# Kernel tuning notes

Measured on AMD Instinct MI355X. Metric: run time of the kernel, lower is better.

Reference implementation:

```python
import jax, jax.numpy as jnp
import numpy as np

LP, LQ, B, D0, H = 128, 128, 64, 150, 150
D = 2 * D0  # in_size after self-concatenation


def setup_inputs() -> dict:
    key = jax.random.key(0)
    ks = jax.random.split(key, 12)
    s = 0.08  # weight scale to keep tanh/sigmoid out of hard saturation
    return {
        "Up": jax.random.normal(ks[0], (LP, B, D0), jnp.float32),
        "Uq": jax.random.normal(ks[1], (LQ, B, D0), jnp.float32),
        "Wp": jax.random.normal(ks[2], (H, D), jnp.float32) * s,
        "Wq": jax.random.normal(ks[3], (H, D), jnp.float32) * s,
        "Wv": jax.random.normal(ks[4], (H, H), jnp.float32) * s,
        "Wg": jax.random.normal(ks[5], (2 * D, 2 * D), jnp.float32) * s,
        "V": jax.random.normal(ks[6], (B, H), jnp.float32) * s,
        "v0": jax.random.normal(ks[7], (B, H), jnp.float32) * s,
        "W_ih": jax.random.normal(ks[8], (3 * H, 2 * D), jnp.float32) * s,
        "W_hh": jax.random.normal(ks[9], (3 * H, H), jnp.float32) * s,
        "b_ih": jax.random.normal(ks[10], (3 * H,), jnp.float32) * s,
        "b_hh": jax.random.normal(ks[11], (3 * H,), jnp.float32) * s,
    }


def reference(Up, Uq, Wp, Wq, Wv, Wg, V, v0, W_ih, W_hh, b_ih, b_hh):
    # self-concat of features, as in the original forward
    Upc = jnp.concatenate([Up, Up], axis=2)  # (LP, B, D)
    Uqc = jnp.concatenate([Uq, Uq], axis=2)  # (LQ, B, D)
    # Wq @ Uq is loop-invariant in the original; hoist it (same math)
    Wuq = jnp.einsum('lbd,hd->lbh', Uqc, Wq)  # (LQ, B, H)

    def step(v, up_i):
        # up_i: (B, D); v: (B, H)
        wup = up_i @ Wp.T                                   # (B, H)
        x = jnp.tanh(wup[None] + Wuq + (v @ Wv.T)[None])    # (LQ, B, H)
        s = jnp.einsum('lbh,bh->bl', x, V)                  # (B, LQ)
        a = jax.nn.softmax(s, axis=1)
        c = jnp.einsum('bl,lbd->bd', a, Uqc)                # (B, D)
        r = jnp.concatenate([up_i, c], axis=1)              # (B, 2D)
        r = jax.nn.sigmoid(r @ Wg.T) * r                    # gated input
        # PyTorch GRUCell math
        gi = r @ W_ih.T + b_ih                              # (B, 3H)
        gh = v @ W_hh.T + b_hh                              # (B, 3H)
        i_r, i_z, i_n = jnp.split(gi, 3, axis=1)
        h_r, h_z, h_n = jnp.split(gh, 3, axis=1)
        rr = jax.nn.sigmoid(i_r + h_r)
        zz = jax.nn.sigmoid(i_z + h_z)
        n = jnp.tanh(i_n + rr * h_n)
        h = (1.0 - zz) * n + zz * v
        return h, h

    _, vs = jax.lax.scan(step, v0, Upc)  # vs: (LP, B, H)
    return vs  # dropout in eval mode = identity
```

## Files before the change

kernel.cpp:

```cpp
#include <hip/hip_runtime.h>
#include <hip/hip_fp16.h>

typedef _Float16 h2_t __attribute__((ext_vector_type(2)));

__device__ __forceinline__ float dot2f(int w, int x, float acc) {
#if __has_builtin(__builtin_amdgcn_fdot2)
  return __builtin_amdgcn_fdot2(__builtin_bit_cast(h2_t, w),
                                __builtin_bit_cast(h2_t, x), acc, false);
#else
  h2_t a = __builtin_bit_cast(h2_t, w);
  h2_t b = __builtin_bit_cast(h2_t, x);
  return acc + (float)a[0] * (float)b[0] + (float)a[1] * (float)b[1];
#endif
}

__device__ __forceinline__ float rcp_f(float x) {
#if __has_builtin(__builtin_amdgcn_rcpf)
  return __builtin_amdgcn_rcpf(x);
#else
  return 1.0f / x;
#endif
}

__device__ __forceinline__ float fast_tanh(float x) {
  float e = exp2f(x * 2.885390082f);
  return 1.0f - 2.0f * rcp_f(e + 1.0f);
}
__device__ __forceinline__ float fast_sigmoid(float x) {
  return rcp_f(1.0f + exp2f(x * -1.442695041f));
}
__device__ __forceinline__ int packh2(float a, float b) {
  h2_t h;
  h[0] = (_Float16)a;
  h[1] = (_Float16)b;
  return __builtin_bit_cast(int, h);
}

__device__ __forceinline__ int ldi_coh(const int* p) {
  return __hip_atomic_load((int*)p, __ATOMIC_RELAXED, __HIP_MEMORY_SCOPE_AGENT);
}
__device__ __forceinline__ float ldf_coh(const float* p) {
  return __hip_atomic_load((float*)p, __ATOMIC_RELAXED,
                           __HIP_MEMORY_SCOPE_AGENT);
}
__device__ __forceinline__ void sti_coh(int* p, int v) {
  __hip_atomic_store(p, v, __ATOMIC_RELAXED, __HIP_MEMORY_SCOPE_AGENT);
}
__device__ __forceinline__ void stf_coh(float* p, float v) {
  __hip_atomic_store(p, v, __ATOMIC_RELAXED, __HIP_MEMORY_SCOPE_AGENT);
}

#define DOTC(W, X, A)                                                          \
  {                                                                            \
    int4 _x = (X);                                                             \
    A = dot2f((W).x, _x.x, A);                                                 \
    A = dot2f((W).y, _x.y, A);                                                 \
    A = dot2f((W).z, _x.z, A);                                                 \
    A = dot2f((W).w, _x.w, A);                                                 \
  }

__global__ void prep_weights(const float* __restrict__ Wp,
                             const float* __restrict__ Wv,
                             const float* __restrict__ Wg,
                             const float* __restrict__ Wih,
                             const float* __restrict__ Whh,
                             __half* __restrict__ oMa, __half* __restrict__ oWg,
                             __half* __restrict__ oWih,
                             __half* __restrict__ oWhh, int* __restrict__ flags,
                             int* __restrict__ payload) {
  if (blockIdx.x == 0) {
    for (int j = threadIdx.x; j < 1024; j += 256) flags[j] = 0;
  }
  int idx = blockIdx.x * 256 + threadIdx.x;
  const int NMa = 150 * 304, NWg = 600 * 304, NWih = 900 * 304,
            NWhh = 452 * 152;
  if (idx < NMa) {
    int r = idx / 304, c = idx % 304;
    float v = 0.f;
    if (c < 150)
      v = Wp[r * 300 + c] + Wp[r * 300 + 150 + c];
    else if (c >= 152 && c < 302)
      v = Wv[r * 150 + (c - 152)];
    oMa[(c >> 3) * 1200 + r * 8 + (c & 7)] = __float2half(v);
    return;
  }
  idx -= NMa;
  if (idx < NWg) {
    int r = idx / 304, c = idx % 304;
    float v = 0.f;
    if (c < 150)
      v = Wg[r * 600 + c] + Wg[r * 600 + 150 + c];
    else if (c >= 152 && c < 302) {
      int d = c - 152;
      v = Wg[r * 600 + 300 + d] + Wg[r * 600 + 450 + d];
    }
    oWg[(c >> 3) * 4800 + r * 8 + (c & 7)] = __float2half(v);
    return;
  }
  idx -= NWg;
  if (idx < NWih) {
    int s = idx / 304, c = idx % 304;
    int r = s >> 1, off = (s & 1) * 300;
    float v = (c < 300) ? Wih[r * 600 + off + c] : 0.f;
    oWih[(c >> 3) * 7200 + s * 8 + (c & 7)] = __float2half(v);
    return;
  }
  idx -= NWih;
  if (idx < NWhh) {
    int r = idx / 152, c = idx % 152;
    float v = (r < 450 && c < 150) ? Whh[r * 150 + c] : 0.f;
    oWhh[(c >> 3) * 3616 + r * 8 + (c & 7)] = __float2half(v);
  }
}

__global__ __launch_bounds__(256) void prep_wuq(const float* __restrict__ Uq,
                                                const float* __restrict__ Wq,
                                                __half* __restrict__ oWuq,
                                                __half* __restrict__ oUqh) {
  __shared__ float sUql[64 * 150];
  const int l = blockIdx.x, tid = threadIdx.x;
  for (int idx = tid; idx < 9600; idx += 256) sUql[idx] = Uq[l * 9600 + idx];
  __syncthreads();
  for (int idx = tid; idx < 64 * 152; idx += 256) {
    int bb = idx / 152, d = idx % 152;
    float v = (d < 150) ? sUql[bb * 150 + d] : 0.f;
    oUqh[(size_t)bb * 19456 + l * 152 + d] = __float2half(v);
  }
  if (tid < 152) {
    const int h = tid;
    if (h < 150) {
      float wq[150];
#pragma unroll
      for (int d = 0; d < 150; ++d)
        wq[d] = Wq[h * 300 + d] + Wq[h * 300 + 150 + d];
      for (int bb = 0; bb < 64; ++bb) {
        float acc = 0.f;
#pragma unroll
        for (int d = 0; d < 150; ++d) acc += wq[d] * sUql[bb * 150 + d];
        oWuq[(size_t)bb * 19456 + l * 152 + h] = __float2half(acc);
      }
    } else {
      for (int bb = 0; bb < 64; ++bb)
        oWuq[(size_t)bb * 19456 + l * 152 + h] = __float2half(0.f);
    }
  }
}

__device__ __forceinline__ void post_and_wait(int* f4, int q, int target) {
  __syncthreads();
  if (threadIdx.x == 0) sti_coh(&f4[q], target);
  if (threadIdx.x < 4) {
    int spins = 0;
    while (ldi_coh(&f4[threadIdx.x]) < target && ++spins < (1 << 20)) {
      __builtin_amdgcn_s_sleep(1);
    }
  }
  __syncthreads();
}

__global__ __launch_bounds__(1024, 1) void pq_main(
    const float* __restrict__ Up, const float* __restrict__ V,
    const float* __restrict__ v0, const float* __restrict__ b_ih,
    const float* __restrict__ b_hh, const int* __restrict__ gWuq,
    const __half* __restrict__ gUqh, const int* __restrict__ gMa,
    const int* __restrict__ gWg, const int* __restrict__ gWih,
    const int* __restrict__ gWhh, int* __restrict__ flags,
    int* __restrict__ payload, float* __restrict__ out) {
  __shared__ __align__(16) float sTV[304];
  __shared__ __align__(16) float sV[152];
  __shared__ __align__(16) float sGh[456];
  __shared__ __align__(16) float sS[128];
  __shared__ __align__(16) float sSS[4];
  __shared__ __align__(16) float sC0[152];
  __shared__ __align__(16) float sCp[608];
  __shared__ __align__(16) float sU[152];
  __shared__ __align__(16) float sv_[152];
  __shared__ __align__(16) int sXd[152];
  __shared__ __align__(16) int svh[76];
  __shared__ __align__(16) int sRgh[304];
  __shared__ __align__(16) float sGi[456];
  __shared__ __align__(16) float sBih[456];
  __shared__ __align__(16) float sBhh[456];
  extern __shared__ __align__(16) int dynlds[];
  int* sWuq = dynlds;
  __half* sUqh = (__half*)(dynlds + 9728);

  const int t = threadIdx.x;
  const int c = blockIdx.x & 63;
  const int q = blockIdx.x >> 6;
  const int b = c;

  int* myflags = flags + c * 16;
  int* pl = payload + c * 4096;
  float* plS = (float*)pl;
  float* plGh = (float*)(pl + 512);
  float* plGi = (float*)(pl + 1024);

  const int4* MaT4 = (const int4*)gMa;
  const int4* WgT4 = (const int4*)gWg;
  const int4* WihT4 = (const int4*)gWih;
  const int4* WhhT4 = (const int4*)gWhh;

  const int baseR = 113 * q - (q == 3 ? 1 : 0);
  const int cntR = (q < 2) ? 113 : 112;
  const int c_lo = (q == 0) ? 0 : (q == 1) ? 18 : (q == 2) ? 38 : 56;
  const int c_hi = (q == 0) ? 18 : (q == 1) ? 37 : (q == 2) ? 56 : 75;

  int4 a0, a1, a2, a3, a4, a5, a6, a7, a8, a9;
  int4 b0, b1, b2, b3, b4, b5, b6, b7, b8, b9;
  {
    const int4* p;
    int nr, sub, step, nch, row;
    if (t < 152) {
      p = MaT4; nr = 150; step = 4; nch = 38;
      sub = t & 3; row = 38 * q + (t >> 2);
      if (row > 149) row = 149;
    } else if (t < 378) {
      p = WhhT4; nr = 452; step = 2; nch = 19;
      int u2 = t - 152; sub = u2 & 1; row = baseR + (u2 >> 1);
    } else if (t >= 384 && t < 984) {
      p = WgT4; nr = 600; step = 4; nch = 38;
      int u2 = t - 384; sub = u2 & 3; row = 150 * q + (u2 >> 2);
    } else {
      p = MaT4; nr = 150; step = 4; nch = 38; sub = 0; row = 0;
    }
#define LDA(i)                                                                 \
  {                                                                            \
    int cc = sub + step * (i);                                                 \
    if (cc > nch - 1) cc = nch - 1;                                            \
    a##i = p[cc * nr + row];                                                   \
  }
    LDA(0) LDA(1) LDA(2) LDA(3) LDA(4) LDA(5) LDA(6) LDA(7) LDA(8) LDA(9)
#undef LDA
  }
  {
    int row = (t < 900) ? (t >> 1) : 0;
    int sub = (t < 900) ? (t & 1) : 0;
#define LDB(i)                                                                 \
  {                                                                            \
    int cq = c_lo + sub + 2 * (i);                                             \
    if (cq > c_hi) cq = c_hi;                                                  \
    int hf = (cq >= 38) ? 1 : 0;                                               \
    int cc = cq - 38 * hf;                                                     \
    b##i = WihT4[cc * 900 + 2 * row + hf];                                     \
  }
    LDB(0) LDB(1) LDB(2) LDB(3) LDB(4) LDB(5) LDB(6) LDB(7) LDB(8) LDB(9)
#undef LDB
  }

  for (int idx = t; idx < 9728; idx += 1024) sWuq[idx] = gWuq[b * 9728 + idx];
  {
    const int* gU2 = (const int*)(gUqh + (size_t)b * 19456);
    int* sU2 = (int*)sUqh;
    for (int idx = t; idx < 9728; idx += 1024) sU2[idx] = gU2[idx];
  }
  if (t < 150) {
    sV[t] = V[b * 150 + t];
    float v_ = v0[b * 150 + t];
    sv_[t] = v_;
    float vn = __shfl_down(v_, 1);
    if (!(t & 1)) svh[t >> 1] = packh2(v_, vn);
    float u_ = Up[b * 150 + t];
    sU[t] = u_;
    float un = __shfl_down(u_, 1);
    if (!(t & 1)) sXd[t >> 1] = packh2(u_, un);
  }
  for (int idx = t; idx < 450; idx += 1024) {
    sBih[idx] = b_ih[idx];
    sBhh[idx] = b_hh[idx];
  }
  if (t < 304) {
    sRgh[t] = 0;
    sTV[t] = 0.f;
  }
  if (t == 0) {
    svh[75] = 0;
    sXd[75] = 0;
    sXd[151] = 0;
    sV[150] = 0.f;
    sV[151] = 0.f;
  }
  const int4* sXd4 = (const int4*)sXd;
  const int4* svh4 = (const int4*)svh;
  const int4* sRgh4 = (const int4*)sRgh;
  const int c_lq = t / 150;
  const int c_d0 = t - c_lq * 150;
  __syncthreads();

#pragma unroll 1
  for (int i = 0; i < 128; ++i) {
    float unext = 0.f;
    if (t >= 640 && t < 790) {
      int ii = (i < 127) ? (i + 1) : 127;
      unext = Up[ii * 9600 + b * 150 + (t - 640)];
    }

    if (t < 152) {
      int rl = t >> 2, sub = t & 3;
      float acc0 = 0.f, acc1 = 0.f;
#define MAD(i2, A)                                                             \
  {                                                                            \
    int cc = sub + 4 * (i2);                                                   \
    if (cc < 38) {                                                             \
      int4 x = (cc < 19) ? sXd4[cc] : svh4[cc - 19];                           \
      DOTC(a##i2, x, A)                                                        \
    }                                                                          \
  }
      MAD(0, acc0) MAD(1, acc1) MAD(2, acc0) MAD(3, acc1) MAD(4, acc0)
      MAD(5, acc1) MAD(6, acc0) MAD(7, acc1) MAD(8, acc0) MAD(9, acc1)
#undef MAD
      float acc = acc0 + acc1;
      acc += __shfl_xor(acc, 1);
      acc += __shfl_xor(acc, 2);
      float accN = __shfl_down(acc, 4);
      if (sub == 0 && !(rl & 1)) {
        int w = 19 * q + (rl >> 1);
        int h = 38 * q + rl;
        float4 tv;
        tv.x = acc;
        tv.y = accN;
        tv.z = sV[h];
        tv.w = sV[h + 1];
        ((float4*)sTV)[w] = tv;
      }
    } else if (t < 378) {
      int u2 = t - 152;
      int rl = u2 >> 1, sub = u2 & 1;
      int r = baseR + rl;
      float acc0 = 0.f, acc1 = 0.f;
#define HHD(i2, A)                                                             \
  {                                                                            \
    int cc = sub + 2 * (i2);                                                   \
    if (cc < 19) DOTC(a##i2, svh4[cc], A)                                      \
  }
      HHD(0, acc0) HHD(1, acc1) HHD(2, acc0) HHD(3, acc1) HHD(4, acc0)
      HHD(5, acc1) HHD(6, acc0) HHD(7, acc1) HHD(8, acc0) HHD(9, acc1)
#undef HHD
      float acc = acc0 + acc1;
      acc += __shfl_xor(acc, 1);
      if (sub == 0 && rl < cntR) stf_coh(&plGh[r], acc + sBhh[r]);
    }
    __syncthreads();

    {
      const int l = t >> 3, sub = t & 7;
      const int base = l * 76;
      float acc = 0.f;
#pragma unroll
      for (int k = 0; k < 3; ++k) {
        int wl = sub + 8 * k;
        if (wl < 19) {
          int w = 19 * q + wl;
          int qq = sWuq[base + w];
          float4 tv = ((const float4*)sTV)[w];
          h2_t hq = __builtin_bit_cast(h2_t, qq);
          float x0 = (float)hq[0] + tv.x;
          float x1 = (float)hq[1] + tv.y;
          acc += fast_tanh(x0) * tv.z;
          acc += fast_tanh(x1) * tv.w;
        }
      }
      acc += __shfl_xor(acc, 1);
      acc += __shfl_xor(acc, 2);
      acc += __shfl_xor(acc, 4);
      if (sub == 0) stf_coh(&plS[128 * q + l], acc);
    }
    post_and_wait(myflags, q, i + 1);
    if (t < 128) {
      float s = ldf_coh(&plS[t]) + ldf_coh(&plS[128 + t]) +
                ldf_coh(&plS[256 + t]) + ldf_coh(&plS[384 + t]);
      sS[t] = exp2f(s * 1.442695041f);
    } else if (t >= 128 && t < 578) {
      sGh[t - 128] = ldf_coh(&plGh[t - 128]);
    }
    __syncthreads();

    if (t < 600) {
      const __half* src = sUqh + c_lq * 32 * 152 + c_d0;
      float acc = 0.f;
#pragma unroll
      for (int j = 0; j < 32; ++j) {
        float a = sS[c_lq * 32 + j];
        acc += a * __half2float(src[j * 152]);
      }
      sCp[c_lq * 152 + c_d0] = acc;
    } else if (t >= 960) {
      int lane = t - 960;
      float e = sS[lane] + sS[64 + lane];
#pragma unroll
      for (int o = 1; o < 64; o <<= 1) e += __shfl_xor(e, o);
      if (lane == 0) sSS[0] = e;
    }
    __syncthreads();
    if (t < 150) {
      float inv = rcp_f(sSS[0]);
      float c0 = (sCp[t] + sCp[152 + t] + sCp[304 + t] + sCp[456 + t]) * inv;
      sC0[t] = c0;
      float cn = __shfl_down(c0, 1);
      if (!(t & 1)) sXd[76 + (t >> 1)] = packh2(c0, cn);
    }
    __syncthreads();

    if (t >= 384 && t < 984) {
      int u2 = t - 384;
      int rl = u2 >> 2, sub = u2 & 3;
      int j = 150 * q + rl;
      float acc0 = 0.f, acc1 = 0.f;
#define WGD(i2, A)                                                             \
  {                                                                            \
    int cc = sub + 4 * (i2);                                                   \
    if (cc < 38) DOTC(a##i2, sXd4[cc], A)                                      \
  }
      WGD(0, acc0) WGD(1, acc1) WGD(2, acc0) WGD(3, acc1) WGD(4, acc0)
      WGD(5, acc1) WGD(6, acc0) WGD(7, acc1) WGD(8, acc0) WGD(9, acc1)
#undef WGD
      float acc = acc0 + acc1;
      acc += __shfl_xor(acc, 1);
      acc += __shfl_xor(acc, 2);
      if (sub == 0) {
        float rb;
        if (j < 150)
          rb = sU[j];
        else if (j < 300)
          rb = sU[j - 150];
        else if (j < 450)
          rb = sC0[j - 300];
        else
          rb = sC0[j - 450];
        float rg = rb * fast_sigmoid(acc);
        ((__half*)sRgh)[(j < 300) ? j : (j + 4)] = __float2half(rg);
      }
    }
    __syncthreads();

    if (t < 900) {
      int row = t >> 1, sub = t & 1;
      float acc0 = 0.f, acc1 = 0.f;
#define IHD(i2, A)                                                             \
  {                                                                            \
    int cq = c_lo + sub + 2 * (i2);                                            \
    if (cq <= c_hi) DOTC(b##i2, sRgh4[cq], A)                                  \
  }
      IHD(0, acc0) IHD(1, acc1) IHD(2, acc0) IHD(3, acc1) IHD(4, acc0)
      IHD(5, acc1) IHD(6, acc0) IHD(7, acc1) IHD(8, acc0) IHD(9, acc1)
#undef IHD
      float acc = acc0 + acc1;
      acc += __shfl_xor(acc, 1);
      if (!sub) stf_coh(&plGi[456 * q + row], acc);
    }
    post_and_wait(myflags + 4, q, i + 1);
    if (t < 450) {
      float g0 = ldf_coh(&plGi[t]);
      float g1 = ldf_coh(&plGi[456 + t]);
      float g2 = ldf_coh(&plGi[912 + t]);
      float g3 = ldf_coh(&plGi[1368 + t]);
      sGi[t] = g0 + g1 + g2 + g3 + sBih[t];
    }
    __syncthreads();

    if (t < 150) {
      float ir = sGi[t], iz = sGi[150 + t], in_ = sGi[300 + t];
      float hr = sGh[t], hz = sGh[150 + t], hn = sGh[300 + t];
      float rr = fast_sigmoid(ir + hr);
      float zz = fast_sigmoid(iz + hz);
      float nn = fast_tanh(in_ + rr * hn);
      float vold = sv_[t];
      float hv = nn + zz * (vold - nn);
      if (q == 0) out[i * 9600 + b * 150 + t] = hv;
      sv_[t] = hv;
      float hv1 = __shfl_down(hv, 1);
      if (!(t & 1)) svh[t >> 1] = packh2(hv, hv1);
    } else if (t >= 640 && t < 790) {
      int t2 = t - 640;
      sU[t2] = unext;
      float un = __shfl_down(unext, 1);
      if (!(t2 & 1)) sXd[t2 >> 1] = packh2(unext, un);
    }
    __syncthreads();
  }
}

extern "C" void kernel_launch(void* const* d_in, const int* in_sizes, int n_in,
                              void* d_out, int out_size, void* d_ws,
                              size_t ws_size, hipStream_t stream) {
  const float* Up = (const float*)d_in[0];
  const float* Uq = (const float*)d_in[1];
  const float* Wp = (const float*)d_in[2];
  const float* Wq = (const float*)d_in[3];
  const float* Wv = (const float*)d_in[4];
  const float* Wg = (const float*)d_in[5];
  const float* V = (const float*)d_in[6];
  const float* v0 = (const float*)d_in[7];
  const float* Wih = (const float*)d_in[8];
  const float* Whh = (const float*)d_in[9];
  const float* bih = (const float*)d_in[10];
  const float* bhh = (const float*)d_in[11];

  char* ws = (char*)d_ws;
  __half* wsWuq = (__half*)(ws);
  __half* wsUqh = (__half*)(ws + 2490368);
  __half* wsMa = (__half*)(ws + 4980736);
  __half* wsWg = (__half*)(ws + 5071936);
  __half* wsWih = (__half*)(ws + 5436736);
  __half* wsWhh = (__half*)(ws + 5983936);
  int* wsFlags = (int*)(ws + 6121472);
  int* wsPayload = (int*)(ws + 6125568);

  (void)hipFuncSetAttribute((const void*)pq_main,
                            hipFuncAttributeMaxDynamicSharedMemorySize, 77824);

  prep_weights<<<2228, 256, 0, stream>>>(Wp, Wv, Wg, Wih, Whh, wsMa, wsWg,
                                         wsWih, wsWhh, wsFlags, wsPayload);
  prep_wuq<<<128, 256, 0, stream>>>(Uq, Wq, wsWuq, wsUqh);
  pq_main<<<256, 1024, 77824, stream>>>(Up, V, v0, bih, bhh, (const int*)wsWuq,
                                        wsUqh, (const int*)wsMa,
                                        (const int*)wsWg, (const int*)wsWih,
                                        (const int*)wsWhh, wsFlags, wsPayload,
                                        (float*)d_out);
}
```

Before: 1.233 ms.

## Replace flag barriers with tagged 64-bit payload slots polled per element

Removes the per-step flag post-and-wait barriers between the four cooperating blocks of each batch. Each partial result is now stored as a 64-bit word carrying the value and a step tag, and consumers poll the specific slots they need until the tag matches. This removes two block-wide syncthreads-plus-spin phases per step, letting consumers start once their own data has arrived. The cost is more coherent global polling traffic and wider payload stores, and the payload buffer must be zeroed in the prep kernel.

```diff
diff --git a/kernel.cpp b/kernel.cpp
--- a/kernel.cpp
+++ b/kernel.cpp
@@ -2,6 +2,7 @@
 #include <hip/hip_fp16.h>
 
 typedef _Float16 h2_t __attribute__((ext_vector_type(2)));
+typedef unsigned long long u64;
 
 __device__ __forceinline__ float dot2f(int w, int x, float acc) {
 #if __has_builtin(__builtin_amdgcn_fdot2)
@@ -36,18 +37,49 @@
   return __builtin_bit_cast(int, h);
 }
 
-__device__ __forceinline__ int ldi_coh(const int* p) {
-  return __hip_atomic_load((int*)p, __ATOMIC_RELAXED, __HIP_MEMORY_SCOPE_AGENT);
-}
-__device__ __forceinline__ float ldf_coh(const float* p) {
-  return __hip_atomic_load((float*)p, __ATOMIC_RELAXED,
-                           __HIP_MEMORY_SCOPE_AGENT);
-}
-__device__ __forceinline__ void sti_coh(int* p, int v) {
+__device__ __forceinline__ u64 ld64_coh(const u64* p) {
+  return __hip_atomic_load((u64*)p, __ATOMIC_RELAXED, __HIP_MEMORY_SCOPE_AGENT);
+}
+__device__ __forceinline__ void st64_coh(u64* p, u64 v) {
   __hip_atomic_store(p, v, __ATOMIC_RELAXED, __HIP_MEMORY_SCOPE_AGENT);
 }
-__device__ __forceinline__ void stf_coh(float* p, float v) {
-  __hip_atomic_store(p, v, __ATOMIC_RELAXED, __HIP_MEMORY_SCOPE_AGENT);
+__device__ __forceinline__ u64 packtv(float v, unsigned tag) {
+  return ((u64)tag << 32) | (u64)__float_as_uint(v);
+}
+__device__ __forceinline__ float slotval(u64 v) {
+  return __uint_as_float((unsigned)v);
+}
+
+__device__ __forceinline__ float poll1(const u64* p, unsigned tag) {
+  u64 v;
+  int spins = 0;
+  for (;;) {
+    v = ld64_coh(p);
+    if ((unsigned)(v >> 32) == tag || ++spins >= (1 << 20)) break;
+    __builtin_amdgcn_s_sleep(1);
+  }
+  return slotval(v);
+}
+__device__ __forceinline__ float poll4(const u64* p0, const u64* p1,
+                                       const u64* p2, const u64* p3,
+                                       unsigned tag) {
+  float acc = 0.f;
+  unsigned got = 0;
+  int spins = 0;
+  while (got != 15u && spins < (1 << 20)) {
+    u64 v0 = 0, v1 = 0, v2 = 0, v3 = 0;
+    if (!(got & 1u)) v0 = ld64_coh(p0);
+    if (!(got & 2u)) v1 = ld64_coh(p1);
+    if (!(got & 4u)) v2 = ld64_coh(p2);
+    if (!(got & 8u)) v3 = ld64_coh(p3);
+    if (!(got & 1u) && (unsigned)(v0 >> 32) == tag) { acc += slotval(v0); got |= 1u; }
+    if (!(got & 2u) && (unsigned)(v1 >> 32) == tag) { acc += slotval(v1); got |= 2u; }
+    if (!(got & 4u) && (unsigned)(v2 >> 32) == tag) { acc += slotval(v2); got |= 4u; }
+    if (!(got & 8u) && (unsigned)(v3 >> 32) == tag) { acc += slotval(v3); got |= 8u; }
+    ++spins;
+    if (got != 15u) __builtin_amdgcn_s_sleep(1);
+  }
+  return acc;
 }
 
 #define DOTC(W, X, A)                                                          \
@@ -66,12 +98,10 @@
                              const float* __restrict__ Whh,
                              __half* __restrict__ oMa, __half* __restrict__ oWg,
                              __half* __restrict__ oWih,
-                             __half* __restrict__ oWhh, int* __restrict__ flags,
+                             __half* __restrict__ oWhh,
                              int* __restrict__ payload) {
-  if (blockIdx.x == 0) {
-    for (int j = threadIdx.x; j < 1024; j += 256) flags[j] = 0;
-  }
   int idx = blockIdx.x * 256 + threadIdx.x;
+  if (idx < 393216) payload[idx] = 0;
   const int NMa = 150 * 304, NWg = 600 * 304, NWih = 900 * 304,
             NWhh = 452 * 152;
   if (idx < NMa) {
@@ -146,26 +176,14 @@
   }
 }
 
-__device__ __forceinline__ void post_and_wait(int* f4, int q, int target) {
-  __syncthreads();
-  if (threadIdx.x == 0) sti_coh(&f4[q], target);
-  if (threadIdx.x < 4) {
-    int spins = 0;
-    while (ldi_coh(&f4[threadIdx.x]) < target && ++spins < (1 << 20)) {
-      __builtin_amdgcn_s_sleep(1);
-    }
-  }
-  __syncthreads();
-}
-
 __global__ __launch_bounds__(1024, 1) void pq_main(
     const float* __restrict__ Up, const float* __restrict__ V,
     const float* __restrict__ v0, const float* __restrict__ b_ih,
     const float* __restrict__ b_hh, const int* __restrict__ gWuq,
     const __half* __restrict__ gUqh, const int* __restrict__ gMa,
     const int* __restrict__ gWg, const int* __restrict__ gWih,
-    const int* __restrict__ gWhh, int* __restrict__ flags,
-    int* __restrict__ payload, float* __restrict__ out) {
+    const int* __restrict__ gWhh, u64* __restrict__ payload,
+    float* __restrict__ out) {
   __shared__ __align__(16) float sTV[304];
   __shared__ __align__(16) float sV[152];
   __shared__ __align__(16) float sGh[456];
@@ -190,11 +208,10 @@
   const int q = blockIdx.x >> 6;
   const int b = c;
 
-  int* myflags = flags + c * 16;
-  int* pl = payload + c * 4096;
-  float* plS = (float*)pl;
-  float* plGh = (float*)(pl + 512);
-  float* plGi = (float*)(pl + 1024);
+  u64* pl = payload + (size_t)c * 3072;
+  u64* sSlot = pl;
+  u64* ghSlot = pl + 512;
+  u64* giSlot = pl + 1024;
 
   const int4* MaT4 = (const int4*)gMa;
   const int4* WgT4 = (const int4*)gWg;
@@ -289,6 +306,7 @@
 
 #pragma unroll 1
   for (int i = 0; i < 128; ++i) {
+    const unsigned tagv = (unsigned)(i + 1);
     float unext = 0.f;
     if (t >= 640 && t < 790) {
       int ii = (i < 127) ? (i + 1) : 127;
@@ -338,7 +356,8 @@
 #undef HHD
       float acc = acc0 + acc1;
       acc += __shfl_xor(acc, 1);
-      if (sub == 0 && rl < cntR) stf_coh(&plGh[r], acc + sBhh[r]);
+      if (sub == 0 && rl < cntR)
+        st64_coh(&ghSlot[r], packtv(acc + sBhh[r], tagv));
     }
     __syncthreads();
 
@@ -363,15 +382,15 @@
       acc += __shfl_xor(acc, 1);
       acc += __shfl_xor(acc, 2);
       acc += __shfl_xor(acc, 4);
-      if (sub == 0) stf_coh(&plS[128 * q + l], acc);
-    }
-    post_and_wait(myflags, q, i + 1);
+      if (sub == 0) st64_coh(&sSlot[128 * q + l], packtv(acc, tagv));
+    }
+
     if (t < 128) {
-      float s = ldf_coh(&plS[t]) + ldf_coh(&plS[128 + t]) +
-                ldf_coh(&plS[256 + t]) + ldf_coh(&plS[384 + t]);
+      float s = poll4(&sSlot[t], &sSlot[128 + t], &sSlot[256 + t],
+                      &sSlot[384 + t], tagv);
       sS[t] = exp2f(s * 1.442695041f);
     } else if (t >= 128 && t < 578) {
-      sGh[t - 128] = ldf_coh(&plGh[t - 128]);
+      sGh[t - 128] = poll1(&ghSlot[t - 128], tagv);
     }
     __syncthreads();
 
@@ -446,15 +465,12 @@
 #undef IHD
       float acc = acc0 + acc1;
       acc += __shfl_xor(acc, 1);
-      if (!sub) stf_coh(&plGi[456 * q + row], acc);
-    }
-    post_and_wait(myflags + 4, q, i + 1);
+      if (!sub) st64_coh(&giSlot[456 * q + row], packtv(acc, tagv));
+    }
     if (t < 450) {
-      float g0 = ldf_coh(&plGi[t]);
-      float g1 = ldf_coh(&plGi[456 + t]);
-      float g2 = ldf_coh(&plGi[912 + t]);
-      float g3 = ldf_coh(&plGi[1368 + t]);
-      sGi[t] = g0 + g1 + g2 + g3 + sBih[t];
+      float g = poll4(&giSlot[t], &giSlot[456 + t], &giSlot[912 + t],
+                      &giSlot[1368 + t], tagv);
+      sGi[t] = g + sBih[t];
     }
     __syncthreads();
 
@@ -503,18 +519,17 @@
   __half* wsWg = (__half*)(ws + 5071936);
   __half* wsWih = (__half*)(ws + 5436736);
   __half* wsWhh = (__half*)(ws + 5983936);
-  int* wsFlags = (int*)(ws + 6121472);
-  int* wsPayload = (int*)(ws + 6125568);
+  u64* wsPayload = (u64*)(ws + 6121472);
 
   (void)hipFuncSetAttribute((const void*)pq_main,
                             hipFuncAttributeMaxDynamicSharedMemorySize, 77824);
 
   prep_weights<<<2228, 256, 0, stream>>>(Wp, Wv, Wg, Wih, Whh, wsMa, wsWg,
-                                         wsWih, wsWhh, wsFlags, wsPayload);
+                                         wsWih, wsWhh, (int*)wsPayload);
   prep_wuq<<<128, 256, 0, stream>>>(Uq, Wq, wsWuq, wsUqh);
   pq_main<<<256, 1024, 77824, stream>>>(Up, V, v0, bih, bhh, (const int*)wsWuq,
                                         wsUqh, (const int*)wsMa,
                                         (const int*)wsWg, (const int*)wsWih,
-                                        (const int*)wsWhh, wsFlags, wsPayload,
+                                        (const int*)wsWhh, wsPayload,
                                         (float*)d_out);
 }
```

Result: slower. 1.458 ms (+18.2%).

## Keep per-thread Wuq and Uq slices in registers instead of dynamic LDS

Applied to the files above, without the earlier changes.

Each thread loads, once at kernel start, exactly the Wuq half2 words and the 32 Uq half values it uses across all 128 steps, and keeps them in registers. The per-step LDS reads in the score and context loops go away, and the 77 KB dynamic shared memory allocation is dropped. The cost is 15 extra live VGPRs per thread in a 1024-thread block that already holds 80 int4 weight registers, so spilling or reduced occupancy is a risk.

```diff
diff --git a/kernel.cpp b/kernel.cpp
--- a/kernel.cpp
+++ b/kernel.cpp
@@ -181,9 +181,6 @@
   __shared__ __align__(16) float sGi[456];
   __shared__ __align__(16) float sBih[456];
   __shared__ __align__(16) float sBhh[456];
-  extern __shared__ __align__(16) int dynlds[];
-  int* sWuq = dynlds;
-  __half* sUqh = (__half*)(dynlds + 9728);
 
   const int t = threadIdx.x;
   const int c = blockIdx.x & 63;
@@ -205,6 +202,9 @@
   const int cntR = (q < 2) ? 113 : 112;
   const int c_lo = (q == 0) ? 0 : (q == 1) ? 18 : (q == 2) ? 38 : 56;
   const int c_hi = (q == 0) ? 18 : (q == 1) ? 37 : (q == 2) ? 56 : 75;
+
+  const int c_lq = t / 150;
+  const int c_d0 = t - c_lq * 150;
 
   int4 a0, a1, a2, a3, a4, a5, a6, a7, a8, a9;
   int4 b0, b1, b2, b3, b4, b5, b6, b7, b8, b9;
@@ -248,12 +248,28 @@
 #undef LDB
   }
 
-  for (int idx = t; idx < 9728; idx += 1024) sWuq[idx] = gWuq[b * 9728 + idx];
+  int w0 = 0, w1 = 0, w2 = 0;
   {
-    const int* gU2 = (const int*)(gUqh + (size_t)b * 19456);
-    int* sU2 = (int*)sUqh;
-    for (int idx = t; idx < 9728; idx += 1024) sU2[idx] = gU2[idx];
-  }
+    const int l = t >> 3, sub = t & 7;
+    const int* src = gWuq + b * 9728 + l * 76 + 19 * q;
+    if (sub < 19) w0 = src[sub];
+    if (sub + 8 < 19) w1 = src[sub + 8];
+    if (sub + 16 < 19) w2 = src[sub + 16];
+  }
+  int4 uq0 = {0, 0, 0, 0}, uq1 = {0, 0, 0, 0}, uq2 = {0, 0, 0, 0},
+       uq3 = {0, 0, 0, 0};
+  if (t < 600) {
+    const unsigned short* us =
+        (const unsigned short*)(gUqh + (size_t)b * 19456 + c_lq * 32 * 152 +
+                                c_d0);
+#define PQ(J) (int)((unsigned)us[(J) * 152] | ((unsigned)us[(J + 1) * 152] << 16))
+    uq0.x = PQ(0);  uq0.y = PQ(2);  uq0.z = PQ(4);  uq0.w = PQ(6);
+    uq1.x = PQ(8);  uq1.y = PQ(10); uq1.z = PQ(12); uq1.w = PQ(14);
+    uq2.x = PQ(16); uq2.y = PQ(18); uq2.z = PQ(20); uq2.w = PQ(22);
+    uq3.x = PQ(24); uq3.y = PQ(26); uq3.z = PQ(28); uq3.w = PQ(30);
+#undef PQ
+  }
+
   if (t < 150) {
     sV[t] = V[b * 150 + t];
     float v_ = v0[b * 150 + t];
@@ -283,8 +299,6 @@
   const int4* sXd4 = (const int4*)sXd;
   const int4* svh4 = (const int4*)svh;
   const int4* sRgh4 = (const int4*)sRgh;
-  const int c_lq = t / 150;
-  const int c_d0 = t - c_lq * 150;
   __syncthreads();
 
 #pragma unroll 1
@@ -343,23 +357,24 @@
     __syncthreads();
 
     {
-      const int l = t >> 3, sub = t & 7;
-      const int base = l * 76;
+      const int sub = t & 7;
+      const int l = t >> 3;
       float acc = 0.f;
-#pragma unroll
-      for (int k = 0; k < 3; ++k) {
-        int wl = sub + 8 * k;
-        if (wl < 19) {
-          int w = 19 * q + wl;
-          int qq = sWuq[base + w];
-          float4 tv = ((const float4*)sTV)[w];
-          h2_t hq = __builtin_bit_cast(h2_t, qq);
-          float x0 = (float)hq[0] + tv.x;
-          float x1 = (float)hq[1] + tv.y;
-          acc += fast_tanh(x0) * tv.z;
-          acc += fast_tanh(x1) * tv.w;
-        }
-      }
+#define BTERM(K, WREG)                                                         \
+  {                                                                            \
+    int wl = sub + 8 * K;                                                      \
+    if (wl < 19) {                                                             \
+      int w = 19 * q + wl;                                                     \
+      float4 tv = ((const float4*)sTV)[w];                                     \
+      h2_t hq = __builtin_bit_cast(h2_t, WREG);                                \
+      float x0 = (float)hq[0] + tv.x;                                          \
+      float x1 = (float)hq[1] + tv.y;                                          \
+      acc += fast_tanh(x0) * tv.z;                                             \
+      acc += fast_tanh(x1) * tv.w;                                             \
+    }                                                                          \
+  }
+      BTERM(0, w0) BTERM(1, w1) BTERM(2, w2)
+#undef BTERM
       acc += __shfl_xor(acc, 1);
       acc += __shfl_xor(acc, 2);
       acc += __shfl_xor(acc, 4);
@@ -376,13 +391,19 @@
     __syncthreads();
 
     if (t < 600) {
-      const __half* src = sUqh + c_lq * 32 * 152 + c_d0;
+      const float* a = sS + c_lq * 32;
       float acc = 0.f;
-#pragma unroll
-      for (int j = 0; j < 32; ++j) {
-        float a = sS[c_lq * 32 + j];
-        acc += a * __half2float(src[j * 152]);
-      }
+#define CT(PK, J)                                                              \
+  {                                                                            \
+    h2_t hp = __builtin_bit_cast(h2_t, PK);                                    \
+    acc += a[J] * (float)hp[0];                                                \
+    acc += a[(J) + 1] * (float)hp[1];                                          \
+  }
+      CT(uq0.x, 0)  CT(uq0.y, 2)  CT(uq0.z, 4)  CT(uq0.w, 6)
+      CT(uq1.x, 8)  CT(uq1.y, 10) CT(uq1.z, 12) CT(uq1.w, 14)
+      CT(uq2.x, 16) CT(uq2.y, 18) CT(uq2.z, 20) CT(uq2.w, 22)
+      CT(uq3.x, 24) CT(uq3.y, 26) CT(uq3.z, 28) CT(uq3.w, 30)
+#undef CT
       sCp[c_lq * 152 + c_d0] = acc;
     } else if (t >= 960) {
       int lane = t - 960;
@@ -506,15 +527,11 @@
   int* wsFlags = (int*)(ws + 6121472);
   int* wsPayload = (int*)(ws + 6125568);
 
-  (void)hipFuncSetAttribute((const void*)pq_main,
-                            hipFuncAttributeMaxDynamicSharedMemorySize, 77824);
-
   prep_weights<<<2228, 256, 0, stream>>>(Wp, Wv, Wg, Wih, Whh, wsMa, wsWg,
                                          wsWih, wsWhh, wsFlags, wsPayload);
   prep_wuq<<<128, 256, 0, stream>>>(Uq, Wq, wsWuq, wsUqh);
-  pq_main<<<256, 1024, 77824, stream>>>(Up, V, v0, bih, bhh, (const int*)wsWuq,
-                                        wsUqh, (const int*)wsMa,
-                                        (const int*)wsWg, (const int*)wsWih,
-                                        (const int*)wsWhh, wsFlags, wsPayload,
-                                        (float*)d_out);
-}
+  pq_main<<<256, 1024, 0, stream>>>(Up, V, v0, bih, bhh, (const int*)wsWuq,
+                                    wsUqh, (const int*)wsMa, (const int*)wsWg,
+                                    (const int*)wsWih, (const int*)wsWhh,
+                                    wsFlags, wsPayload, (float*)d_out);
+}
```

Result: slower. 2.335 ms (+89.3%).

## Fuse context partial reduction via shuffles and replace syncthreads with lean barriers

Applied to the files above, without the earlier changes.

The context-vector computation now gives each d four lanes, one per LQ quarter, and reduces them with warp shuffles. This removes the sCp scratch buffer and one full block barrier per step. The softmax denominator is folded into the exp stage using two wave-level sums. The padded Uq layout in LDS (stride 2436) is meant to avoid bank conflicts for the new access pattern. All __syncthreads calls become an inline s_waitcnt lgkmcnt(0)+s_barrier, which skips waiting on outstanding global memory ops and relies on the coherent loads and stores being ordered correctly some other way.

```diff
diff --git a/kernel.cpp b/kernel.cpp
--- a/kernel.cpp
+++ b/kernel.cpp
@@ -2,6 +2,9 @@
 #include <hip/hip_fp16.h>
 
 typedef _Float16 h2_t __attribute__((ext_vector_type(2)));
+
+#define BAR_LGKM() \
+  asm volatile("s_waitcnt lgkmcnt(0)\n\ts_barrier" ::: "memory")
 
 __device__ __forceinline__ float dot2f(int w, int x, float acc) {
 #if __has_builtin(__builtin_amdgcn_fdot2)
@@ -155,7 +158,7 @@
       __builtin_amdgcn_s_sleep(1);
     }
   }
-  __syncthreads();
+  BAR_LGKM();
 }
 
 __global__ __launch_bounds__(1024, 1) void pq_main(
@@ -172,7 +175,6 @@
   __shared__ __align__(16) float sS[128];
   __shared__ __align__(16) float sSS[4];
   __shared__ __align__(16) float sC0[152];
-  __shared__ __align__(16) float sCp[608];
   __shared__ __align__(16) float sU[152];
   __shared__ __align__(16) float sv_[152];
   __shared__ __align__(16) int sXd[152];
@@ -252,7 +254,10 @@
   {
     const int* gU2 = (const int*)(gUqh + (size_t)b * 19456);
     int* sU2 = (int*)sUqh;
-    for (int idx = t; idx < 9728; idx += 1024) sU2[idx] = gU2[idx];
+    for (int idx = t; idx < 9728; idx += 1024) {
+      int lq = idx / 2432, rem = idx - lq * 2432;
+      sU2[lq * 2436 + rem] = gU2[idx];
+    }
   }
   if (t < 150) {
     sV[t] = V[b * 150 + t];
@@ -283,8 +288,6 @@
   const int4* sXd4 = (const int4*)sXd;
   const int4* svh4 = (const int4*)svh;
   const int4* sRgh4 = (const int4*)sRgh;
-  const int c_lq = t / 150;
-  const int c_d0 = t - c_lq * 150;
   __syncthreads();
 
 #pragma unroll 1
@@ -340,7 +343,7 @@
       acc += __shfl_xor(acc, 1);
       if (sub == 0 && rl < cntR) stf_coh(&plGh[r], acc + sBhh[r]);
     }
-    __syncthreads();
+    BAR_LGKM();
 
     {
       const int l = t >> 3, sub = t & 7;
@@ -369,37 +372,38 @@
     if (t < 128) {
       float s = ldf_coh(&plS[t]) + ldf_coh(&plS[128 + t]) +
                 ldf_coh(&plS[256 + t]) + ldf_coh(&plS[384 + t]);
-      sS[t] = exp2f(s * 1.442695041f);
+      float e = exp2f(s * 1.442695041f);
+      sS[t] = e;
+      float es = e;
+#pragma unroll
+      for (int o = 1; o < 64; o <<= 1) es += __shfl_xor(es, o);
+      if (t == 0) sSS[0] = es;
+      if (t == 64) sSS[1] = es;
     } else if (t >= 128 && t < 578) {
       sGh[t - 128] = ldf_coh(&plGh[t - 128]);
     }
-    __syncthreads();
+    BAR_LGKM();
 
     if (t < 600) {
-      const __half* src = sUqh + c_lq * 32 * 152 + c_d0;
+      const int d = t >> 2, lq = t & 3;
+      const __half* src = sUqh + lq * 4872 + d;
+      const float* a = sS + lq * 32;
       float acc = 0.f;
 #pragma unroll
       for (int j = 0; j < 32; ++j) {
-        float a = sS[c_lq * 32 + j];
-        acc += a * __half2float(src[j * 152]);
+        acc += a[j] * __half2float(src[j * 152]);
       }
-      sCp[c_lq * 152 + c_d0] = acc;
-    } else if (t >= 960) {
-      int lane = t - 960;
-      float e = sS[lane] + sS[64 + lane];
-#pragma unroll
-      for (int o = 1; o < 64; o <<= 1) e += __shfl_xor(e, o);
-      if (lane == 0) sSS[0] = e;
-    }
-    __syncthreads();
-    if (t < 150) {
-      float inv = rcp_f(sSS[0]);
-      float c0 = (sCp[t] + sCp[152 + t] + sCp[304 + t] + sCp[456 + t]) * inv;
-      sC0[t] = c0;
-      float cn = __shfl_down(c0, 1);
-      if (!(t & 1)) sXd[76 + (t >> 1)] = packh2(c0, cn);
-    }
-    __syncthreads();
+      acc += __shfl_xor(acc, 1);
+      acc += __shfl_xor(acc, 2);
+      float inv = rcp_f(sSS[0] + sSS[1]);
+      float c0 = acc * inv;
+      float cn = __shfl_down(c0, 4);
+      if (lq == 0) {
+        sC0[d] = c0;
+        if (!(d & 1)) sXd[76 + (d >> 1)] = packh2(c0, cn);
+      }
+    }
+    BAR_LGKM();
 
     if (t >= 384 && t < 984) {
       int u2 = t - 384;
@@ -431,7 +435,7 @@
         ((__half*)sRgh)[(j < 300) ? j : (j + 4)] = __float2half(rg);
       }
     }
-    __syncthreads();
+    BAR_LGKM();
 
     if (t < 900) {
       int row = t >> 1, sub = t & 1;
@@ -456,7 +460,7 @@
       float g3 = ldf_coh(&plGi[1368 + t]);
       sGi[t] = g0 + g1 + g2 + g3 + sBih[t];
     }
-    __syncthreads();
+    BAR_LGKM();
 
     if (t < 150) {
       float ir = sGi[t], iz = sGi[150 + t], in_ = sGi[300 + t];
@@ -476,7 +480,7 @@
       float un = __shfl_down(unext, 1);
       if (!(t2 & 1)) sXd[t2 >> 1] = packh2(unext, un);
     }
-    __syncthreads();
+    BAR_LGKM();
   }
 }
 
@@ -507,12 +511,12 @@
   int* wsPayload = (int*)(ws + 6125568);
 
   (void)hipFuncSetAttribute((const void*)pq_main,
-                            hipFuncAttributeMaxDynamicSharedMemorySize, 77824);
+                            hipFuncAttributeMaxDynamicSharedMemorySize, 77888);
 
   prep_weights<<<2228, 256, 0, stream>>>(Wp, Wv, Wg, Wih, Whh, wsMa, wsWg,
                                          wsWih, wsWhh, wsFlags, wsPayload);
   prep_wuq<<<128, 256, 0, stream>>>(Uq, Wq, wsWuq, wsUqh);
-  pq_main<<<256, 1024, 77824, stream>>>(Up, V, v0, bih, bhh, (const int*)wsWuq,
+  pq_main<<<256, 1024, 77888, stream>>>(Up, V, v0, bih, bhh, (const int*)wsWuq,
                                         wsUqh, (const int*)wsMa,
                                         (const int*)wsWg, (const int*)wsWih,
                                         (const int*)wsWhh, wsFlags, wsPayload,
```

Measured after the change: 1.291 ms. +4.7%, slower.
